# Performance work log

Hardware: AMD Instinct MI355X
Metric: run time of the kernel (lower is better)

## Reference

```python
import jax, jax.numpy as jnp
import numpy as np

N_ITER = 3


def squash(v):
    # v: [..., out_C]; scale by ||v||^2/(1+||v||^2) and normalize by ||v||
    sq = jnp.sum(v * v, axis=-1, keepdims=True)
    return (sq / (1.0 + sq)) * v / jnp.sqrt(sq)


def setup_inputs() -> dict:
    key = jax.random.key(0)
    k1, k2 = jax.random.split(key)
    B, n_nodes, n_caps, in_C, out_C = 64, 2048, 32, 16, 32
    x = jax.random.normal(k1, (B, n_nodes, in_C), dtype=jnp.float32)
    route_weights = 0.1 * jax.random.normal(k2, (n_nodes, n_caps, in_C, out_C), dtype=jnp.float32)
    return {"x": x, "route_weights": route_weights}


def reference(x, route_weights):
    # priors: [B, n_nodes, n_caps, out_C]
    priors = jnp.einsum('bni,nkio->bnko', x, route_weights)
    logits = jnp.zeros_like(priors)
    outputs = None
    for i in range(N_ITER):
        probs = jax.nn.softmax(logits, axis=2)            # over n_caps
        s = jnp.sum(probs * priors, axis=1, keepdims=True)  # [B,1,n_caps,out_C]
        outputs = squash(s)
        if i != N_ITER - 1:
            delta = jnp.sum(priors * outputs, axis=-1, keepdims=True)
            logits = logits + delta
    return outputs
```

## Files before the change

### kernel.cpp

```cpp
#include <hip/hip_runtime.h>
#include <math.h>


#define BATCH 64
#define NN    2048
#define NK    32
#define NI    16
#define NO    32

#define PNB   16
#define NSETS (NN / PNB)

typedef __bf16 bf16x8 __attribute__((ext_vector_type(8)));
typedef float  f32x16 __attribute__((ext_vector_type(16)));

__device__ __forceinline__ unsigned short f2bf(float f) {
    unsigned int x = __float_as_uint(f);
    unsigned int lsb = (x >> 16) & 1u;
    x += 0x7fffu + lsb;
    return (unsigned short)(x >> 16);
}
__device__ __forceinline__ float bflo(unsigned int u) { return __uint_as_float(u << 16); }
__device__ __forceinline__ float bfhi(unsigned int u) { return __uint_as_float(u & 0xffff0000u); }


__global__ __launch_bounds__(1024) void zero_kernel(float* __restrict__ p) {
    p[blockIdx.x * 1024 + threadIdx.x] = 0.f;
}

__global__ __launch_bounds__(256) void xt_kernel(const float* __restrict__ xg,
                                                 unsigned short* __restrict__ xT) {
    int id = blockIdx.x * 256 + threadIdx.x;
    int b = id >> 13;
    int rem = id & 8191;
    int n = rem >> 2;
    int i4 = rem & 3;
    float4 v = *(const float4*)(xg + ((size_t)b * NN + n) * NI + i4 * 4);
    ushort4 o;
    o.x = f2bf(v.x); o.y = f2bf(v.y); o.z = f2bf(v.z); o.w = f2bf(v.w);
    *(ushort4*)(xT + ((size_t)n * BATCH + b) * NI + i4 * 4) = o;
}

__global__ __launch_bounds__(256) void wqt_kernel(const float* __restrict__ Wg,
                                                  unsigned short* __restrict__ wq) {
    const int w    = threadIdx.x >> 6;
    const int lane = threadIdx.x & 63;
    const int task = blockIdx.x * 4 + w;
    const int o  = lane & 31;
    const int ih = lane >> 5;
    const float* src = Wg + (size_t)task * (NI * NO);
    unsigned short d[8];
#pragma unroll
    for (int j = 0; j < 8; ++j)
        d[j] = f2bf(src[(ih * 8 + j) * NO + o]);
    *(uint4*)(wq + (size_t)task * (NO * NI) + o * NI + ih * 8) = *(uint4*)d;
}

template <int PASS>
__global__ __launch_bounds__(1024) void fused_pass(
    const unsigned short* __restrict__ xT,
    const unsigned short* __restrict__ wq,
    const float* __restrict__ outv,
    float* __restrict__ logits0,
    float* __restrict__ s_glob)
{
    __shared__ float delta_lds[2][32 * 33];

    const int tid  = threadIdx.x;
    const int w    = tid >> 6;
    const int lane = tid & 63;
    const int l5   = lane & 31;
    const int h5   = lane >> 5;
    const int set  = blockIdx.x;
    const int hb   = blockIdx.y;
    const int k0   = 2 * w, k1 = 2 * w + 1;
    const int gb5  = hb * 32 + l5;
    const int sb   = tid >> 5;
    const int sk   = tid & 31;
    const int nbase = set * PNB;

    unsigned orp0[8], orp1[8];
    if constexpr (PASS >= 1) {
#pragma unroll
        for (int q = 0; q < 8; ++q) {
            const int oA = ((2*q) & 3) + 8 * ((2*q) >> 2) + 4 * h5;
            const int oB = ((2*q+1) & 3) + 8 * ((2*q+1) >> 2) + 4 * h5;
            float a0 = outv[(k0 * NO + oA) * BATCH + gb5];
            float b0 = outv[(k0 * NO + oB) * BATCH + gb5];
            float a1 = outv[(k1 * NO + oA) * BATCH + gb5];
            float b1 = outv[(k1 * NO + oB) * BATCH + gb5];
            orp0[q] = (unsigned)f2bf(a0) | ((unsigned)f2bf(b0) << 16);
            orp1[q] = (unsigned)f2bf(a1) | ((unsigned)f2bf(b1) << 16);
        }
    }

    float sa0[16], sa1[16];
#pragma unroll
    for (int r = 0; r < 16; ++r) { sa0[r] = 0.f; sa1[r] = 0.f; }

    bf16x8 aN, b0N, b1N;
    float gN = 0.f;
    {
        const int n = nbase;
        b0N = *(const bf16x8*)(wq + (size_t)n * (NK * NO * NI) + k0 * (NO * NI) + l5 * NI + h5 * 8);
        b1N = *(const bf16x8*)(wq + (size_t)n * (NK * NO * NI) + k1 * (NO * NI) + l5 * NI + h5 * 8);
        aN  = *(const bf16x8*)(xT + (size_t)n * (BATCH * NI) + gb5 * NI + h5 * 8);
        if constexpr (PASS == 2)
            gN = logits0[(size_t)n * (BATCH * NK) + hb * 1024 + tid];
    }

    int buf = 0;
    for (int j = 0; j < PNB; ++j) {
        const int n = nbase + j;
        const bf16x8 aC = aN, b0C = b0N, b1C = b1N;
        const float gC = gN;
        if (j < PNB - 1) {
            const int n2 = n + 1;
            b0N = *(const bf16x8*)(wq + (size_t)n2 * (NK * NO * NI) + k0 * (NO * NI) + l5 * NI + h5 * 8);
            b1N = *(const bf16x8*)(wq + (size_t)n2 * (NK * NO * NI) + k1 * (NO * NI) + l5 * NI + h5 * 8);
            aN  = *(const bf16x8*)(xT + (size_t)n2 * (BATCH * NI) + gb5 * NI + h5 * 8);
            if constexpr (PASS == 2)
                gN = logits0[(size_t)n2 * (BATCH * NK) + hb * 1024 + tid];
        }

        f32x16 c0, c1;
#pragma unroll
        for (int r = 0; r < 16; ++r) { c0[r] = 0.f; c1[r] = 0.f; }
        c0 = __builtin_amdgcn_mfma_f32_32x32x16_bf16(b0C, aC, c0, 0, 0, 0);
        c1 = __builtin_amdgcn_mfma_f32_32x32x16_bf16(b1C, aC, c1, 0, 0, 0);

        if constexpr (PASS == 0) {
#pragma unroll
            for (int r = 0; r < 16; ++r) { sa0[r] += c0[r]; sa1[r] += c1[r]; }
        } else {
            float d0 = 0.f, d1 = 0.f;
#pragma unroll
            for (int r = 0; r < 16; ++r) {
                const unsigned u0 = orp0[r >> 1], u1 = orp1[r >> 1];
                const float o0 = (r & 1) ? bfhi(u0) : bflo(u0);
                const float o1 = (r & 1) ? bfhi(u1) : bflo(u1);
                d0 = fmaf(c0[r], o0, d0);
                d1 = fmaf(c1[r], o1, d1);
            }
            d0 += __shfl_xor(d0, 32);
            d1 += __shfl_xor(d1, 32);

            delta_lds[buf][l5 * 33 + (h5 ? k1 : k0)] = h5 ? d1 : d0;
            __syncthreads();

            float l = delta_lds[buf][sb * 33 + sk];
            if constexpr (PASS == 1)
                logits0[(size_t)n * (BATCH * NK) + hb * 1024 + tid] = l;
            else
                l += gC;
            float e = __expf(l);
            float s = e;
#pragma unroll
            for (int mask = 1; mask < 32; mask <<= 1)
                s += __shfl_xor(s, mask);
            delta_lds[buf][sb * 33 + sk] = e / s;
            __syncthreads();

            const float p0 = delta_lds[buf][l5 * 33 + k0];
            const float p1 = delta_lds[buf][l5 * 33 + k1];
#pragma unroll
            for (int r = 0; r < 16; ++r) {
                sa0[r] = fmaf(p0, c0[r], sa0[r]);
                sa1[r] = fmaf(p1, c1[r], sa1[r]);
            }
            buf ^= 1;
        }
    }

    const float scale = (PASS == 0) ? (1.f / NK) : 1.f;
#pragma unroll
    for (int r = 0; r < 16; ++r) {
        const int o = (r & 3) + 8 * (r >> 2) + 4 * h5;
        atomicAdd(&s_glob[(k0 * NO + o) * BATCH + gb5], sa0[r] * scale);
        atomicAdd(&s_glob[(k1 * NO + o) * BATCH + gb5], sa1[r] * scale);
    }
}

template <int FINAL>
__global__ __launch_bounds__(1024) void reduce_squash2(
    float* __restrict__ s_glob,
    float* __restrict__ outv,
    float* __restrict__ outp)
{
    __shared__ float red[2048];
    __shared__ float coef[64];
    const int k = blockIdx.x;
    const int t = threadIdx.x;
    const int o = t >> 6;
    const int b = t & 63;
    float* base = s_glob + k * 2048;
    float va = base[o * 64 + b];
    float vb = base[(o + 16) * 64 + b];
    base[o * 64 + b] = 0.f;
    base[(o + 16) * 64 + b] = 0.f;
    red[o * 64 + b] = va * va;
    red[(o + 16) * 64 + b] = vb * vb;
    __syncthreads();
    if (t < 64) {
        float sq = 0.f;
#pragma unroll
        for (int oo = 0; oo < 32; ++oo) sq += red[oo * 64 + t];
        coef[t] = sq / ((1.f + sq) * sqrtf(sq));
    }
    __syncthreads();
    const float cf = coef[b];
    if (FINAL) {
        outp[b * 1024 + k * 32 + o]      = va * cf;
        outp[b * 1024 + k * 32 + o + 16] = vb * cf;
    } else {
        outv[k * 2048 + o * 64 + b]        = va * cf;
        outv[k * 2048 + (o + 16) * 64 + b] = vb * cf;
    }
}


#define LBB 32
#define LNCHUNK 8
#define LNBLK (NN / LNCHUNK)
#define LTHREADS 512
#define WK_STRIDE 516

template <int PASS>
__global__ __launch_bounds__(LTHREADS, 1) void legacy_pass(
    const float* __restrict__ xg, const float* __restrict__ Wg,
    const float* __restrict__ outvL, float* __restrict__ logits,
    float* __restrict__ partial)
{
    __shared__ float w_lds[NK * WK_STRIDE];
    __shared__ float x_lds[LBB][NI + 1];
    __shared__ float delta_lds[LBB][NK + 1];
    const int t = threadIdx.x, nb = blockIdx.x, bg = blockIdx.y;
    const int b0 = bg * LBB;
    const int k = t >> 4, bq = t & 15, bl0 = bq * 2, bl1 = bq * 2 + 1;
    float acc0[NO], acc1[NO];
#pragma unroll
    for (int o = 0; o < NO; ++o) { acc0[o] = 0.f; acc1[o] = 0.f; }
    float outr0[NO], outr1[NO];
    if constexpr (PASS >= 1) {
        const float4* o0 = (const float4*)&outvL[((b0 + bl0) * NK + k) * NO];
        const float4* o1 = (const float4*)&outvL[((b0 + bl1) * NK + k) * NO];
#pragma unroll
        for (int q = 0; q < NO / 4; ++q) {
            float4 a = o0[q]; float4 b = o1[q];
            outr0[4*q+0]=a.x; outr0[4*q+1]=a.y; outr0[4*q+2]=a.z; outr0[4*q+3]=a.w;
            outr1[4*q+0]=b.x; outr1[4*q+1]=b.y; outr1[4*q+2]=b.z; outr1[4*q+3]=b.w;
        }
    }
    for (int j = 0; j < LNCHUNK; ++j) {
        const int n = nb * LNCHUNK + j;
        __syncthreads();
        {
            const float4* src = (const float4*)(Wg + (size_t)n * (NK * NI * NO));
#pragma unroll
            for (int r = 0; r < (NK * NI * NO / 4) / LTHREADS; ++r) {
                int idx4 = t + r * LTHREADS;
                float4 v = src[idx4];
                int e = idx4 * 4, kk = e >> 9, rem = e & 511;
                *(float4*)&w_lds[kk * WK_STRIDE + rem] = v;
            }
        }
        { int bl = t >> 4, i = t & 15;
          x_lds[bl][i] = xg[((size_t)(b0 + bl) * NN + n) * NI + i]; }
        __syncthreads();
        if constexpr (PASS == 0) {
#pragma unroll
            for (int i = 0; i < NI; ++i) {
                float xa = x_lds[bl0][i], xb = x_lds[bl1][i];
                const float* wrow = &w_lds[k * WK_STRIDE + i * NO];
#pragma unroll
                for (int o = 0; o < NO; ++o) {
                    float w = wrow[o];
                    acc0[o] = fmaf(xa, w, acc0[o]);
                    acc1[o] = fmaf(xb, w, acc1[o]);
                }
            }
        } else {
            float pr0[NO], pr1[NO];
#pragma unroll
            for (int o = 0; o < NO; ++o) { pr0[o] = 0.f; pr1[o] = 0.f; }
#pragma unroll
            for (int i = 0; i < NI; ++i) {
                float xa = x_lds[bl0][i], xb = x_lds[bl1][i];
                const float* wrow = &w_lds[k * WK_STRIDE + i * NO];
#pragma unroll
                for (int o = 0; o < NO; ++o) {
                    float w = wrow[o];
                    pr0[o] = fmaf(xa, w, pr0[o]);
                    pr1[o] = fmaf(xb, w, pr1[o]);
                }
            }
            float d0 = 0.f, d1 = 0.f;
#pragma unroll
            for (int o = 0; o < NO; ++o) {
                d0 = fmaf(pr0[o], outr0[o], d0);
                d1 = fmaf(pr1[o], outr1[o], d1);
            }
            float l0 = d0, l1 = d1;
            const size_t li0 = ((size_t)(b0 + bl0) * NN + n) * NK + k;
            const size_t li1 = ((size_t)(b0 + bl1) * NN + n) * NK + k;
            if constexpr (PASS == 2) { l0 += logits[li0]; l1 += logits[li1]; }
            else { logits[li0] = d0; logits[li1] = d1; }
            delta_lds[bl0][k] = l0; delta_lds[bl1][k] = l1;
            __syncthreads();
            float m0 = -1e30f, m1 = -1e30f;
#pragma unroll
            for (int kk = 0; kk < NK; ++kk) {
                m0 = fmaxf(m0, delta_lds[bl0][kk]);
                m1 = fmaxf(m1, delta_lds[bl1][kk]);
            }
            float s0 = 0.f, s1 = 0.f;
#pragma unroll
            for (int kk = 0; kk < NK; ++kk) {
                s0 += __expf(delta_lds[bl0][kk] - m0);
                s1 += __expf(delta_lds[bl1][kk] - m1);
            }
            float p0 = __expf(l0 - m0) / s0;
            float p1 = __expf(l1 - m1) / s1;
#pragma unroll
            for (int o = 0; o < NO; ++o) {
                acc0[o] = fmaf(p0, pr0[o], acc0[o]);
                acc1[o] = fmaf(p1, pr1[o], acc1[o]);
            }
        }
    }
    const float scale = (PASS == 0) ? (1.f / NK) : 1.f;
    float4* p0 = (float4*)&partial[(((size_t)nb * BATCH + (b0 + bl0)) * NK + k) * NO];
    float4* p1 = (float4*)&partial[(((size_t)nb * BATCH + (b0 + bl1)) * NK + k) * NO];
#pragma unroll
    for (int q = 0; q < NO / 4; ++q) {
        float4 v0, v1;
        v0.x = acc0[4*q+0]*scale; v0.y = acc0[4*q+1]*scale;
        v0.z = acc0[4*q+2]*scale; v0.w = acc0[4*q+3]*scale;
        v1.x = acc1[4*q+0]*scale; v1.y = acc1[4*q+1]*scale;
        v1.z = acc1[4*q+2]*scale; v1.w = acc1[4*q+3]*scale;
        p0[q] = v0; p1[q] = v1;
    }
}

__global__ __launch_bounds__(256) void legacy_reduce(
    const float* __restrict__ partial, float* __restrict__ outf)
{
    const int tid = blockIdx.x * 256 + threadIdx.x;
    float v = 0.f;
    for (int nb = 0; nb < LNBLK; ++nb)
        v += partial[(size_t)nb * (BATCH * NK * NO) + tid];
    float sq = v * v;
#pragma unroll
    for (int off = 1; off < 32; off <<= 1) sq += __shfl_xor(sq, off);
    float coef = sq / ((1.f + sq) * sqrtf(sq));
    outf[tid] = v * coef;
}


extern "C" void kernel_launch(void* const* d_in, const int* in_sizes, int n_in,
                              void* d_out, int out_size, void* d_ws, size_t ws_size,
                              hipStream_t stream)
{
    const float* xg = (const float*)d_in[0];
    const float* Wg = (const float*)d_in[1];
    float* outp = (float*)d_out;
    char* ws = (char*)d_ws;

    const size_t SZ_WQ     = (size_t)NN * NK * NO * NI * 2;
    const size_t SZ_XT     = (size_t)NN * BATCH * NI * 2;
    const size_t SZ_LOGITS = (size_t)NN * BATCH * NK * 4;
    const size_t SZ_SG     = (size_t)NK * NO * BATCH * 4;
    const size_t SZ_OUTV   = (size_t)NK * NO * BATCH * 4;
    const size_t NEED = SZ_WQ + SZ_XT + SZ_LOGITS + SZ_SG + SZ_OUTV;

    if (ws_size >= NEED) {
        unsigned short* wq = (unsigned short*)ws;
        unsigned short* xT = (unsigned short*)(ws + SZ_WQ);
        float* logits0 = (float*)(ws + SZ_WQ + SZ_XT);
        float* s_glob  = (float*)(ws + SZ_WQ + SZ_XT + SZ_LOGITS);
        float* outv    = (float*)(ws + SZ_WQ + SZ_XT + SZ_LOGITS + SZ_SG);

        zero_kernel<<<64, 1024, 0, stream>>>(s_glob);
        xt_kernel<<<2048, 256, 0, stream>>>(xg, xT);
        wqt_kernel<<<16384, 256, 0, stream>>>(Wg, wq);

        dim3 pg(NSETS, 2);
        fused_pass<0><<<pg, 1024, 0, stream>>>(xT, wq, nullptr, nullptr, s_glob);
        reduce_squash2<0><<<32, 1024, 0, stream>>>(s_glob, outv, nullptr);
        fused_pass<1><<<pg, 1024, 0, stream>>>(xT, wq, outv, logits0, s_glob);
        reduce_squash2<0><<<32, 1024, 0, stream>>>(s_glob, outv, nullptr);
        fused_pass<2><<<pg, 1024, 0, stream>>>(xT, wq, outv, logits0, s_glob);
        reduce_squash2<1><<<32, 1024, 0, stream>>>(s_glob, nullptr, outp);
    } else {
        float* partial = (float*)ws;
        float* logits = (float*)(ws + (size_t)LNBLK * BATCH * NK * NO * 4);
        float* outvL = (float*)(ws + (size_t)LNBLK * BATCH * NK * NO * 4 + (size_t)BATCH * NN * NK * 4);
        dim3 grid(LNBLK, BATCH / LBB);
        const int rblocks = BATCH * NK * NO / 256;
        legacy_pass<0><<<grid, LTHREADS, 0, stream>>>(xg, Wg, nullptr, logits, partial);
        legacy_reduce<<<rblocks, 256, 0, stream>>>(partial, outvL);
        legacy_pass<1><<<grid, LTHREADS, 0, stream>>>(xg, Wg, outvL, logits, partial);
        legacy_reduce<<<rblocks, 256, 0, stream>>>(partial, outvL);
        legacy_pass<2><<<grid, LTHREADS, 0, stream>>>(xg, Wg, outvL, logits, partial);
        legacy_reduce<<<rblocks, 256, 0, stream>>>(partial, outp);
    }
}
```

Before: 380.2 us.

## Compute routing softmax in registers with one barrier and partial-sum exchange

The per-node softmax over capsules no longer round-trips the transposed delta through LDS with two barriers. Each lane now exponentiates its own two logits in place, each wave writes a per-batch partial sum of exponentials, and after a single barrier lanes read 16 partials with float4 loads and normalise. The logits buffer is relaid as [n][k][b] so each lane stores and loads its own values directly. PNB is also halved, which doubles the grid and the number of atomic adds. The trade-off is no max subtraction in the softmax and more atomic traffic.

Result: slower. 1.069 ms (+181.2%).

```diff
diff --git a/kernel.cpp b/kernel.cpp
--- a/kernel.cpp
+++ b/kernel.cpp
@@ -8,8 +8,9 @@
 #define NI    16
 #define NO    32
 
-#define PNB   16
+#define PNB   8
 #define NSETS (NN / PNB)
+#define ESTR  20
 
 typedef __bf16 bf16x8 __attribute__((ext_vector_type(8)));
 typedef float  f32x16 __attribute__((ext_vector_type(16)));
@@ -64,7 +65,7 @@
     float* __restrict__ logits0,
     float* __restrict__ s_glob)
 {
-    __shared__ float delta_lds[2][32 * 33];
+    __shared__ float esum[2][32 * ESTR];
 
     const int tid  = threadIdx.x;
     const int w    = tid >> 6;
@@ -75,8 +76,6 @@
     const int hb   = blockIdx.y;
     const int k0   = 2 * w, k1 = 2 * w + 1;
     const int gb5  = hb * 32 + l5;
-    const int sb   = tid >> 5;
-    const int sk   = tid & 31;
     const int nbase = set * PNB;
 
     unsigned orp0[8], orp1[8];
@@ -99,28 +98,32 @@
     for (int r = 0; r < 16; ++r) { sa0[r] = 0.f; sa1[r] = 0.f; }
 
     bf16x8 aN, b0N, b1N;
-    float gN = 0.f;
+    float gN0 = 0.f, gN1 = 0.f;
     {
         const int n = nbase;
         b0N = *(const bf16x8*)(wq + (size_t)n * (NK * NO * NI) + k0 * (NO * NI) + l5 * NI + h5 * 8);
         b1N = *(const bf16x8*)(wq + (size_t)n * (NK * NO * NI) + k1 * (NO * NI) + l5 * NI + h5 * 8);
         aN  = *(const bf16x8*)(xT + (size_t)n * (BATCH * NI) + gb5 * NI + h5 * 8);
-        if constexpr (PASS == 2)
-            gN = logits0[(size_t)n * (BATCH * NK) + hb * 1024 + tid];
+        if constexpr (PASS == 2) {
+            gN0 = logits0[(size_t)n * (NK * BATCH) + k0 * BATCH + gb5];
+            gN1 = logits0[(size_t)n * (NK * BATCH) + k1 * BATCH + gb5];
+        }
     }
 
     int buf = 0;
     for (int j = 0; j < PNB; ++j) {
         const int n = nbase + j;
         const bf16x8 aC = aN, b0C = b0N, b1C = b1N;
-        const float gC = gN;
+        const float gC0 = gN0, gC1 = gN1;
         if (j < PNB - 1) {
             const int n2 = n + 1;
             b0N = *(const bf16x8*)(wq + (size_t)n2 * (NK * NO * NI) + k0 * (NO * NI) + l5 * NI + h5 * 8);
             b1N = *(const bf16x8*)(wq + (size_t)n2 * (NK * NO * NI) + k1 * (NO * NI) + l5 * NI + h5 * 8);
             aN  = *(const bf16x8*)(xT + (size_t)n2 * (BATCH * NI) + gb5 * NI + h5 * 8);
-            if constexpr (PASS == 2)
-                gN = logits0[(size_t)n2 * (BATCH * NK) + hb * 1024 + tid];
+            if constexpr (PASS == 2) {
+                gN0 = logits0[(size_t)n2 * (NK * BATCH) + k0 * BATCH + gb5];
+                gN1 = logits0[(size_t)n2 * (NK * BATCH) + k1 * BATCH + gb5];
+            }
         }
 
         f32x16 c0, c1;
@@ -145,24 +148,28 @@
             d0 += __shfl_xor(d0, 32);
             d1 += __shfl_xor(d1, 32);
 
-            delta_lds[buf][l5 * 33 + (h5 ? k1 : k0)] = h5 ? d1 : d0;
+            float l0, l1;
+            if constexpr (PASS == 1) {
+                l0 = d0; l1 = d1;
+                if (h5 == 0) {
+                    logits0[(size_t)n * (NK * BATCH) + k0 * BATCH + gb5] = d0;
+                    logits0[(size_t)n * (NK * BATCH) + k1 * BATCH + gb5] = d1;
+                }
+            } else {
+                l0 = gC0 + d0;
+                l1 = gC1 + d1;
+            }
+            const float e0 = __expf(l0), e1 = __expf(l1);
+            if (h5 == 0)
+                esum[buf][l5 * ESTR + w] = e0 + e1;
             __syncthreads();
 
-            float l = delta_lds[buf][sb * 33 + sk];
-            if constexpr (PASS == 1)
-                logits0[(size_t)n * (BATCH * NK) + hb * 1024 + tid] = l;
-            else
-                l += gC;
-            float e = __expf(l);
-            float s = e;
-#pragma unroll
-            for (int mask = 1; mask < 32; mask <<= 1)
-                s += __shfl_xor(s, mask);
-            delta_lds[buf][sb * 33 + sk] = e / s;
-            __syncthreads();
-
-            const float p0 = delta_lds[buf][l5 * 33 + k0];
-            const float p1 = delta_lds[buf][l5 * 33 + k1];
+            const float4* er = (const float4*)&esum[buf][l5 * ESTR];
+            float4 A = er[0], B = er[1], C = er[2], D = er[3];
+            const float es = ((A.x + A.y) + (A.z + A.w)) + ((B.x + B.y) + (B.z + B.w))
+                           + ((C.x + C.y) + (C.z + C.w)) + ((D.x + D.y) + (D.z + D.w));
+            const float inv = __fdividef(1.f, es);
+            const float p0 = e0 * inv, p1 = e1 * inv;
 #pragma unroll
             for (int r = 0; r < 16; ++r) {
                 sa0[r] = fmaf(p0, c0[r], sa0[r]);
@@ -368,7 +375,7 @@
 
     const size_t SZ_WQ     = (size_t)NN * NK * NO * NI * 2;
     const size_t SZ_XT     = (size_t)NN * BATCH * NI * 2;
-    const size_t SZ_LOGITS = (size_t)NN * BATCH * NK * 4;
+    const size_t SZ_LOGITS = (size_t)NN * NK * BATCH * 4;
     const size_t SZ_SG     = (size_t)NK * NO * BATCH * 4;
     const size_t SZ_OUTV   = (size_t)NK * NO * BATCH * 4;
     const size_t NEED = SZ_WQ + SZ_XT + SZ_LOGITS + SZ_SG + SZ_OUTV;
```
